# Kernel tuning notes

Measured on AMD Instinct MI355X. Metric: run time of the kernel, lower is better.

## Reference

```python
import jax, jax.numpy as jnp
import numpy as np

B, T, V, F, O, K_ORDER = 16, 16, 512, 64, 64, 3


def setup_inputs() -> dict:
    key = jax.random.key(0)
    k1, k2, k3, k4 = jax.random.split(key, 4)
    x = jax.random.normal(k1, (B, T, V, F), dtype=jnp.float32)
    Att = jax.random.uniform(k2, (B, V, V), dtype=jnp.float32)
    S = jax.random.uniform(k3, (B, T, V, V), dtype=jnp.float32)
    Theta = jax.random.uniform(k4, (K_ORDER, F, O), dtype=jnp.float32) * 0.1
    return {"x": x, "Att": Att, "S": S, "Theta": Theta}


def reference(x, Att, S, Theta):
    # x: (B,T,V,F); Att: (B,V,V); S: (B,T,V,V); Theta: (k,F,O)
    Bv, Tv, Vv, Fv = x.shape
    k_order = Theta.shape[0]
    # symmetrize via elementwise min with transpose over the two vertex dims
    S = jnp.minimum(S, jnp.swapaxes(S, -1, -2))
    # per-timestep: D = diag(sum(A, axis=1)) (sum over rows, i.e. axis=2 here)
    deg = S.sum(axis=2)                      # (B,T,V)
    eye = jnp.eye(Vv, dtype=x.dtype)
    # L_t = D - A - I
    L_t = deg[..., None] * eye - S - eye     # (B,T,V,V)
    Att_b = Att[:, None]                     # (B,1,V,V) broadcast over T

    # Chebyshev recurrence is ELEMENTWISE in the original code: T_k = 2*L_t*T_{k-1} - T_{k-2}
    Tkm2 = jnp.broadcast_to(eye, L_t.shape)  # T_0 = I
    Tkm1 = L_t                               # T_1 = L_t
    # rhs = (T_k * Att)^T @ x  ->  sum_u (T_k*Att)[u,v] * x[u,f]; then @ Theta[k]
    out = jnp.einsum('btuv,btuf,fo->btvo', Tkm2 * Att_b, x, Theta[0])
    if k_order > 1:
        out = out + jnp.einsum('btuv,btuf,fo->btvo', Tkm1 * Att_b, x, Theta[1])
    for i in range(2, k_order):
        Tk = 2.0 * L_t * Tkm1 - Tkm2
        out = out + jnp.einsum('btuv,btuf,fo->btvo', Tk * Att_b, x, Theta[i])
        Tkm2, Tkm1 = Tkm1, Tk
    return jax.nn.relu(out)                  # (B,T,V,O)
```

## Files before the change

kernel.cpp:

```cpp
#include <hip/hip_runtime.h>

#define VV 512
#define FF 64
#define OO 64
#define YELEMS 8388608

#define C1_OFF    0u
#define C2_OFF    67108864u
#define Y1F8_OFF  134217728u
#define Y2F8_OFF  142606336u
#define YVO_OFF   150994944u
#define DEGP_OFF  201326592u
#define SDG_OFF   205520896u
#define ADG_OFF   206045184u
#define WS_NEED   206569472u

using f32x4  = __attribute__((ext_vector_type(4))) float;
using f32x16 = __attribute__((ext_vector_type(16))) float;
using s16x8  = __attribute__((ext_vector_type(8))) short;
using s16x4  = __attribute__((ext_vector_type(4))) short;
using u16x4  = __attribute__((ext_vector_type(4))) unsigned short;
using i64x2  = __attribute__((ext_vector_type(2))) long;

__device__ __forceinline__ short f2bf(float f) {
    union { float f; unsigned int u; } v; v.f = f;
    unsigned int u = v.u;
    u += 0x7fffu + ((u >> 16) & 1u);
    return (short)(u >> 16);
}
__device__ __forceinline__ float bf2f(unsigned short u) {
    union { unsigned int u; float f; } v; v.u = ((unsigned int)u) << 16; return v.f;
}
__device__ __forceinline__ int swz(int row) { return (row >> 1) & 7; }

__device__ __forceinline__ void gload16(const void* g, void* l) {
    __builtin_amdgcn_global_load_lds(
        (const __attribute__((address_space(1))) unsigned int*)g,
        (__attribute__((address_space(3))) unsigned int*)l, 16, 0, 0);
}

__global__ __launch_bounds__(256, 3)
void coef_kernel(const float* __restrict__ S, const float* __restrict__ Att,
                 unsigned char* __restrict__ ws)
{
    __shared__ float Sij[64][65];
    __shared__ float Sji[64][65];
    __shared__ short Aij[64][68];
    __shared__ short Aji[64][68];

    const int tid = threadIdx.x;
    const int bt = blockIdx.x / 36;
    int p = blockIdx.x - bt * 36;
    int i = 0;
    while (p >= 8 - i) { p -= 8 - i; ++i; }
    const int j = i + p;
    const int b = bt >> 4;
    const int u0i = i * 64, u0j = j * 64;

    const float* Sbt = S + (size_t)bt * VV * VV;
    const float* Abt = Att + (size_t)b * VV * VV;

    {
        const int r = tid >> 2, c4 = (tid & 3) * 16;
        const float* gij = Sbt + (size_t)(u0i + r) * VV + u0j + c4;
        const float* gji = Sbt + (size_t)(u0j + r) * VV + u0i + c4;
        const float* aij = Abt + (size_t)(u0i + r) * VV + u0j + c4;
        const float* aji = Abt + (size_t)(u0j + r) * VV + u0i + c4;
        #pragma unroll
        for (int w = 0; w < 4; ++w) {
            float4 t = ((const float4*)gij)[w];
            Sij[r][c4 + w * 4 + 0] = t.x; Sij[r][c4 + w * 4 + 1] = t.y;
            Sij[r][c4 + w * 4 + 2] = t.z; Sij[r][c4 + w * 4 + 3] = t.w;
        }
        #pragma unroll
        for (int w = 0; w < 4; ++w) {
            float4 t = ((const float4*)gji)[w];
            Sji[r][c4 + w * 4 + 0] = t.x; Sji[r][c4 + w * 4 + 1] = t.y;
            Sji[r][c4 + w * 4 + 2] = t.z; Sji[r][c4 + w * 4 + 3] = t.w;
        }
        #pragma unroll
        for (int w = 0; w < 4; ++w) {
            float4 t = ((const float4*)aij)[w];
            s16x4 pk = { f2bf(t.x), f2bf(t.y), f2bf(t.z), f2bf(t.w) };
            *(s16x4*)&Aij[r][c4 + w * 4] = pk;
        }
        #pragma unroll
        for (int w = 0; w < 4; ++w) {
            float4 t = ((const float4*)aji)[w];
            s16x4 pk = { f2bf(t.x), f2bf(t.y), f2bf(t.z), f2bf(t.w) };
            *(s16x4*)&Aji[r][c4 + w * 4] = pk;
        }
    }
    if (i == j && tid < 64) {
        const int vg = u0i + tid;
        ((float*)(ws + SDG_OFF))[(size_t)bt * VV + vg] = Sbt[(size_t)vg * VV + vg];
        ((float*)(ws + ADG_OFF))[(size_t)bt * VV + vg] = Abt[(size_t)vg * VV + vg];
    }
    __syncthreads();

    unsigned char* c1w = ws + C1_OFF + (size_t)bt * (VV * VV);
    unsigned char* c2w = ws + C2_OFF + (size_t)bt * (VV * VV);
    float* degpW = (float*)(ws + DEGP_OFF) + (size_t)bt * 8 * VV;

    const int v  = tid >> 2;
    const int sp = tid & 3;
    const int pr = sp >> 1, idx = sp & 1;

    #pragma unroll
    for (int pass = 0; pass < 2; ++pass) {
        if (pass == 1 && i == j) break;
        const float (*Tuv)[65] = (pass == 0) ? Sij : Sji;
        const float (*Tvu)[65] = (pass == 0) ? Sji : Sij;
        const short (*Auv)[68] = (pass == 0) ? Aij : Aji;
        const int I = (pass == 0) ? i : j;
        const int J = (pass == 0) ? j : i;
        const bool dtile = (i == j);

        float degp = 0.f;
        int w1[4], w2[4];
        #pragma unroll
        for (int t = 0; t < 2; ++t) {
            const int sl = idx * 4 + t * 2 + pr;
            float c1v[8], c2v[8];
            #pragma unroll
            for (int e = 0; e < 8; ++e) {
                const int u = sl * 8 + e;
                float sm = fminf(Tuv[u][v], Tvu[v][u]);
                float a  = bf2f((unsigned short)Auv[u][v]);
                degp += sm;
                float c1 = -a * sm;
                float c2 = (a + a) * (sm * sm);
                if (dtile && (u == v)) { c1 = 0.f; c2 = 0.f; }
                c1v[e] = c1; c2v[e] = c2;
            }
            int a0 = __builtin_amdgcn_cvt_pk_fp8_f32(c1v[0], c1v[1], 0, false);
            a0     = __builtin_amdgcn_cvt_pk_fp8_f32(c1v[2], c1v[3], a0, true);
            int a1 = __builtin_amdgcn_cvt_pk_fp8_f32(c1v[4], c1v[5], 0, false);
            a1     = __builtin_amdgcn_cvt_pk_fp8_f32(c1v[6], c1v[7], a1, true);
            int b0 = __builtin_amdgcn_cvt_pk_fp8_f32(c2v[0], c2v[1], 0, false);
            b0     = __builtin_amdgcn_cvt_pk_fp8_f32(c2v[2], c2v[3], b0, true);
            int b1 = __builtin_amdgcn_cvt_pk_fp8_f32(c2v[4], c2v[5], 0, false);
            b1     = __builtin_amdgcn_cvt_pk_fp8_f32(c2v[6], c2v[7], b1, true);
            w1[t * 2] = a0; w1[t * 2 + 1] = a1;
            w2[t * 2] = b0; w2[t * 2 + 1] = b1;
        }
        const int vglob = J * 64 + v;
        const size_t rowoff = (size_t)vglob * VV + pr * 256 + I * 32 + idx * 16;
        int4 s1 = { w1[0], w1[1], w1[2], w1[3] };
        int4 s2 = { w2[0], w2[1], w2[2], w2[3] };
        *(int4*)(c1w + rowoff) = s1;
        *(int4*)(c2w + rowoff) = s2;

        degp += __shfl_xor(degp, 1);
        degp += __shfl_xor(degp, 2);
        if (sp == 0) degpW[(size_t)I * VV + vglob] = degp;
    }
}

__global__ __launch_bounds__(256, 4)
void y_kernel2(const float* __restrict__ x, const float* __restrict__ Theta,
               unsigned char* __restrict__ ws)
{
    __shared__ __align__(16) unsigned char smem[32768];
    short* xT = (short*)(smem);

    const int tid = threadIdx.x, lane = tid & 63, q = tid >> 6;
    const int g = lane >> 4, nbase = lane & 15;
    const int bt = blockIdx.x >> 3;
    const int u0 = (blockIdx.x & 7) * 64;

    {
        const float* xp = x + ((size_t)(bt * VV + u0 + lane)) * FF + q * 16;
        float4 a0 = ((const float4*)xp)[0];
        float4 a1 = ((const float4*)xp)[1];
        float4 a2 = ((const float4*)xp)[2];
        float4 a3 = ((const float4*)xp)[3];
        float v[16] = {a0.x,a0.y,a0.z,a0.w, a1.x,a1.y,a1.z,a1.w,
                       a2.x,a2.y,a2.z,a2.w, a3.x,a3.y,a3.z,a3.w};
        s16x8 p0, p1;
        #pragma unroll
        for (int e = 0; e < 8; ++e) { p0[e] = f2bf(v[e]); p1[e] = f2bf(v[8 + e]); }
        const int fs = swz(lane);
        *(s16x8*)&xT[lane * 64 + (((q * 2)     ^ fs) * 8)] = p0;
        *(s16x8*)&xT[lane * 64 + (((q * 2 + 1) ^ fs) * 8)] = p1;
    }
    #pragma unroll
    for (int k = 0; k < 3; ++k) {
        short* tk = (short*)(smem + 8192 + k * 8192);
        s16x8 p0, p1;
        #pragma unroll
        for (int e = 0; e < 8; ++e) {
            p0[e] = f2bf(Theta[k * FF * OO + (q * 16 + e) * OO + lane]);
            p1[e] = f2bf(Theta[k * FF * OO + (q * 16 + 8 + e) * OO + lane]);
        }
        const int fs = swz(lane);
        *(s16x8*)&tk[lane * 64 + (((q * 2)     ^ fs) * 8)] = p0;
        *(s16x8*)&tk[lane * 64 + (((q * 2 + 1) ^ fs) * 8)] = p1;
    }
    __syncthreads();

    f32x4 zero = {0.f, 0.f, 0.f, 0.f};
    f32x4 acc[3][4];
    #pragma unroll
    for (int k = 0; k < 3; ++k)
        #pragma unroll
        for (int nt = 0; nt < 4; ++nt) acc[k][nt] = zero;

    const int mrow = q * 16 + nbase;
    const int moff = mrow * 64, ms = swz(mrow);
    #pragma unroll
    for (int kk = 0; kk < 2; ++kk) {
        const int slotA = kk * 4 + g;
        s16x8 a = *(const s16x8*)&xT[moff + ((slotA ^ ms) * 8)];
        #pragma unroll
        for (int nt = 0; nt < 4; ++nt) {
            const int nrow = nt * 16 + nbase;
            const int nad = nrow * 64 + ((slotA ^ swz(nrow)) * 8);
            #pragma unroll
            for (int k = 0; k < 3; ++k) {
                s16x8 bb = *(const s16x8*)&((short*)(smem + 8192 + k * 8192))[nad];
                acc[k][nt] = __builtin_amdgcn_mfma_f32_16x16x32_bf16(a, bb, acc[k][nt], 0, 0, 0);
            }
        }
    }
    unsigned short* yvo = (unsigned short*)(ws + YVO_OFF);
    unsigned char* y1f8 = ws + Y1F8_OFF + (size_t)bt * 32768;
    unsigned char* y2f8 = ws + Y2F8_OFF + (size_t)bt * 32768;
    #pragma unroll
    for (int k = 0; k < 3; ++k) {
        #pragma unroll
        for (int nt = 0; nt < 4; ++nt) {
            const int o = nt * 16 + nbase;
            const int u = u0 + q * 16 + g * 4;
            #pragma unroll
            for (int r = 0; r < 4; ++r)
                yvo[(size_t)k * YELEMS + (size_t)bt * 32768 + (size_t)(u + r) * OO + o] =
                    (unsigned short)f2bf(acc[k][nt][r]);
            if (k >= 1) {
                const int s = u >> 3;
                const int sw = (s & ~15) | ((s & 15) ^ (o & 15));
                const int ad = o * 512 + sw * 8 + (u & 4);
                int w = __builtin_amdgcn_cvt_pk_fp8_f32(acc[k][nt][0], acc[k][nt][1], 0, false);
                w     = __builtin_amdgcn_cvt_pk_fp8_f32(acc[k][nt][2], acc[k][nt][3], w, true);
                if (k == 1) *(int*)(y1f8 + ad) = w;
                else        *(int*)(y2f8 + ad) = w;
            }
        }
    }
}

__global__ __launch_bounds__(256, 2)
void cheb_b(const unsigned char* __restrict__ ws, float* __restrict__ out)
{
    __shared__ __align__(16) unsigned char yLds[65536];

    const int tid = threadIdx.x, lane = tid & 63;
    const int wv = tid >> 6;
    const int vh = wv >> 1, oh = wv & 1;
    const int rl = lane & 31, hi = lane >> 5;

    const int wg = blockIdx.x;
    const int bt = (wg & 7) + ((wg >> 6) << 3);
    const int vt = (wg >> 3) & 7;
    const int v0 = vt * 64;

    {
        const unsigned char* y1img = ws + Y1F8_OFF + (size_t)bt * 32768;
        const unsigned char* y2img = ws + Y2F8_OFF + (size_t)bt * 32768;
        const int wo = wv * 1024 + lane * 16;
        #pragma unroll
        for (int i = 0; i < 8; ++i) {
            gload16(y1img + i * 4096 + wo, (char*)yLds + i * 4096 + wv * 1024);
            gload16(y2img + i * 4096 + wo, (char*)yLds + 32768 + i * 4096 + wv * 1024);
        }
    }

    const size_t crow = (size_t)(v0 + vh * 32 + rl) * VV + hi * 256;
    const unsigned char* c1base = ws + C1_OFF + (size_t)bt * (VV * VV) + crow;
    const unsigned char* c2base = ws + C2_OFF + (size_t)bt * (VV * VV) + crow;
    i64x2 c1p[16], c2p[16];
    #pragma unroll
    for (int jj = 0; jj < 16; ++jj) {
        c1p[jj] = *(const i64x2*)(c1base + jj * 16);
        c2p[jj] = *(const i64x2*)(c2base + jj * 16);
    }

    __syncthreads();

    f32x16 acc;
    #pragma unroll
    for (int i = 0; i < 16; ++i) acc[i] = 0.f;

    const int yrow = (oh * 32 + rl) * 512;
    const int x15  = rl & 15;

    #pragma unroll
    for (int it = 0; it < 32; ++it) {
        const long a1 = c1p[it >> 1][it & 1];
        const long a2 = c2p[it >> 1][it & 1];
        const int s  = it * 2 + hi;
        const int sw = (s & ~15) | ((s & 15) ^ x15);
        const int ad = yrow + sw * 8;
        const long b1 = *(const long*)&yLds[ad];
        const long b2 = *(const long*)&yLds[32768 + ad];
        acc = __builtin_amdgcn_mfma_f32_32x32x16_fp8_fp8(a1, b1, acc, 0, 0, 0);
        acc = __builtin_amdgcn_mfma_f32_32x32x16_fp8_fp8(a2, b2, acc, 0, 0, 0);
    }

    __syncthreads();
    {
        float* ep = (float*)yLds;
        const float* degp = (const float*)(ws + DEGP_OFF) + (size_t)bt * 8 * VV;
        const float* SdgW = (const float*)(ws + SDG_OFF) + (size_t)bt * VV;
        const float* AdgW = (const float*)(ws + ADG_OFF) + (size_t)bt * VV;
        if (tid < 64) {
            float dv = 0.f;
            #pragma unroll
            for (int s = 0; s < 8; ++s) dv += degp[(size_t)s * VV + v0 + tid];
            ep[tid] = dv;
        } else if (tid < 128) {
            ep[64 + (tid - 64)] = SdgW[v0 + (tid - 64)];
        } else if (tid < 192) {
            ep[128 + (tid - 128)] = AdgW[v0 + (tid - 128)];
        }
    }
    __syncthreads();

    const float* ep = (const float*)yLds;
    const unsigned short* yvo = (const unsigned short*)(ws + YVO_OFF) + (size_t)bt * 32768;
    float* obt = out + (size_t)bt * VV * OO;
    const int o = oh * 32 + rl;

    #pragma unroll
    for (int r = 0; r < 16; ++r) {
        const int vloc = vh * 32 + (r & 3) + 8 * (r >> 2) + 4 * hi;
        const int vgr = v0 + vloc;
        const float dv = ep[vloc];
        const float Sd = ep[64 + vloc];
        const float Ad = ep[128 + vloc];
        const float Ld = dv - Sd - 1.0f;
        const float w1 = Ad * Ld;
        const float w2 = Ad * (2.0f * Ld * Ld - 1.0f);
        const size_t yi = (size_t)vgr * OO + o;
        float y0v = bf2f(yvo[yi]);
        float y1v = bf2f(yvo[(size_t)YELEMS + yi]);
        float y2v = bf2f(yvo[(size_t)2 * YELEMS + yi]);
        float val = acc[r] + Ad * y0v + w1 * y1v + w2 * y2v;
        obt[(size_t)vgr * OO + o] = fmaxf(val, 0.0f);
    }
}

__global__ __launch_bounds__(256, 4)
void y_kernel_fb(const float* __restrict__ x, const float* __restrict__ Theta,
                 unsigned short* __restrict__ yT)
{
    __shared__ __align__(16) unsigned char smem[32768];
    short* xT = (short*)(smem);
    const int tid = threadIdx.x, lane = tid & 63, q = tid >> 6;
    const int g = lane >> 4, nbase = lane & 15;
    const int bt = blockIdx.x >> 3;
    const int u0 = (blockIdx.x & 7) * 64;
    {
        const float* xp = x + ((size_t)(bt * VV + u0 + lane)) * FF + q * 16;
        float4 a0 = ((const float4*)xp)[0];
        float4 a1 = ((const float4*)xp)[1];
        float4 a2 = ((const float4*)xp)[2];
        float4 a3 = ((const float4*)xp)[3];
        float v[16] = {a0.x,a0.y,a0.z,a0.w, a1.x,a1.y,a1.z,a1.w,
                       a2.x,a2.y,a2.z,a2.w, a3.x,a3.y,a3.z,a3.w};
        s16x8 p0, p1;
        #pragma unroll
        for (int e = 0; e < 8; ++e) { p0[e] = f2bf(v[e]); p1[e] = f2bf(v[8 + e]); }
        const int fs = swz(lane);
        *(s16x8*)&xT[lane * 64 + (((q * 2)     ^ fs) * 8)] = p0;
        *(s16x8*)&xT[lane * 64 + (((q * 2 + 1) ^ fs) * 8)] = p1;
    }
    #pragma unroll
    for (int k = 0; k < 3; ++k) {
        short* tk = (short*)(smem + 8192 + k * 8192);
        s16x8 p0, p1;
        #pragma unroll
        for (int e = 0; e < 8; ++e) {
            p0[e] = f2bf(Theta[k * FF * OO + (q * 16 + e) * OO + lane]);
            p1[e] = f2bf(Theta[k * FF * OO + (q * 16 + 8 + e) * OO + lane]);
        }
        const int fs = swz(lane);
        *(s16x8*)&tk[lane * 64 + (((q * 2)     ^ fs) * 8)] = p0;
        *(s16x8*)&tk[lane * 64 + (((q * 2 + 1) ^ fs) * 8)] = p1;
    }
    __syncthreads();
    f32x4 zero = {0.f, 0.f, 0.f, 0.f};
    f32x4 acc[3][4];
    #pragma unroll
    for (int k = 0; k < 3; ++k)
        #pragma unroll
        for (int nt = 0; nt < 4; ++nt) acc[k][nt] = zero;
    const int mrow = q * 16 + nbase;
    const int moff = mrow * 64, ms = swz(mrow);
    #pragma unroll
    for (int kk = 0; kk < 2; ++kk) {
        const int slotA = kk * 4 + g;
        s16x8 a = *(const s16x8*)&xT[moff + ((slotA ^ ms) * 8)];
        #pragma unroll
        for (int nt = 0; nt < 4; ++nt) {
            const int nrow = nt * 16 + nbase;
            const int nad = nrow * 64 + ((slotA ^ swz(nrow)) * 8);
            #pragma unroll
            for (int k = 0; k < 3; ++k) {
                s16x8 bb = *(const s16x8*)&((short*)(smem + 8192 + k * 8192))[nad];
                acc[k][nt] = __builtin_amdgcn_mfma_f32_16x16x32_bf16(a, bb, acc[k][nt], 0, 0, 0);
            }
        }
    }
    #pragma unroll
    for (int k = 0; k < 3; ++k) {
        #pragma unroll
        for (int nt = 0; nt < 4; ++nt) {
            const int o = nt * 16 + nbase;
            const int u = u0 + q * 16 + g * 4;
            u16x4 pk;
            #pragma unroll
            for (int r = 0; r < 4; ++r) pk[r] = (unsigned short)f2bf(acc[k][nt][r]);
            *(u16x4*)&yT[(size_t)k * YELEMS + ((size_t)(bt * 64 + o)) * VV + u] = pk;
        }
    }
}

__global__ __launch_bounds__(256, 4)
void cheb_main_fb(const float* __restrict__ S, const float* __restrict__ Att,
                  const unsigned short* __restrict__ yT, float* __restrict__ out)
{
    const int tid = threadIdx.x, lane = tid & 63, q = tid >> 6;
    const int g = lane >> 4, nbase = lane & 15;
    const int wg = blockIdx.x;
    const int bt = (wg & 7) + ((wg >> 6) << 3);
    const int vt = (wg >> 3) & 7;
    const int v0 = vt * 64;
    const int b  = bt >> 4;
    const float* Sbt = S + (size_t)bt * VV * VV;
    const float* Abt = Att + (size_t)b * VV * VV;
    const unsigned short* y0g = yT + (size_t)bt * 64 * VV;
    const unsigned short* y1g = y0g + (size_t)YELEMS;
    const unsigned short* y2g = y0g + (size_t)2 * YELEMS;
    const int mrow = q * 16 + nbase;
    const int vg   = v0 + mrow;
    const float* Srow = Sbt + (size_t)vg * VV;
    const float* Scol = Sbt + vg;
    const float* Acol = Abt + vg;
    f32x4 zero = {0.f, 0.f, 0.f, 0.f};
    f32x4 acc[4];
    #pragma unroll
    for (int i = 0; i < 4; ++i) acc[i] = zero;
    float da0 = 0.f, da1 = 0.f, adg = 0.f, sdg = 0.f;
    #pragma unroll
    for (int ut = 0; ut < 8; ++ut) {
        const int u0t = ut * 64;
        #pragma unroll
        for (int kk = 0; kk < 2; ++kk) {
            const int ub = u0t + (kk * 4 + g) * 8;
            s16x8 b10 = *(const s16x8*)&y1g[(size_t)(0 * 16 + nbase) * VV + ub];
            s16x8 b11 = *(const s16x8*)&y1g[(size_t)(1 * 16 + nbase) * VV + ub];
            s16x8 b12 = *(const s16x8*)&y1g[(size_t)(2 * 16 + nbase) * VV + ub];
            s16x8 b13 = *(const s16x8*)&y1g[(size_t)(3 * 16 + nbase) * VV + ub];
            f32x4 r0 = *(const f32x4*)(Srow + ub);
            f32x4 r1 = *(const f32x4*)(Srow + ub + 4);
            s16x8 a1, a2;
            #pragma unroll
            for (int e = 0; e < 8; ++e) {
                float sc = Scol[(size_t)(ub + e) * VV];
                float av = Acol[(size_t)(ub + e) * VV];
                float rv = (e < 4) ? r0[e] : r1[e - 4];
                float sm = fminf(sc, rv);
                if (e & 1) da1 += sm; else da0 += sm;
                float c1 = -av * sm;
                float c2 = (av + av) * (sm * sm);
                if (ub + e == vg) { c1 = 0.f; c2 = 0.f; adg = av; sdg = sm; }
                a1[e] = f2bf(c1);
                a2[e] = f2bf(c2);
            }
            acc[0] = __builtin_amdgcn_mfma_f32_16x16x32_bf16(a1, b10, acc[0], 0, 0, 0);
            acc[1] = __builtin_amdgcn_mfma_f32_16x16x32_bf16(a1, b11, acc[1], 0, 0, 0);
            acc[2] = __builtin_amdgcn_mfma_f32_16x16x32_bf16(a1, b12, acc[2], 0, 0, 0);
            acc[3] = __builtin_amdgcn_mfma_f32_16x16x32_bf16(a1, b13, acc[3], 0, 0, 0);
            s16x8 b20 = *(const s16x8*)&y2g[(size_t)(0 * 16 + nbase) * VV + ub];
            s16x8 b21 = *(const s16x8*)&y2g[(size_t)(1 * 16 + nbase) * VV + ub];
            s16x8 b22 = *(const s16x8*)&y2g[(size_t)(2 * 16 + nbase) * VV + ub];
            s16x8 b23 = *(const s16x8*)&y2g[(size_t)(3 * 16 + nbase) * VV + ub];
            acc[0] = __builtin_amdgcn_mfma_f32_16x16x32_bf16(a2, b20, acc[0], 0, 0, 0);
            acc[1] = __builtin_amdgcn_mfma_f32_16x16x32_bf16(a2, b21, acc[1], 0, 0, 0);
            acc[2] = __builtin_amdgcn_mfma_f32_16x16x32_bf16(a2, b22, acc[2], 0, 0, 0);
            acc[3] = __builtin_amdgcn_mfma_f32_16x16x32_bf16(a2, b23, acc[3], 0, 0, 0);
        }
    }
    float da = da0 + da1;
    da  += __shfl_xor(da, 16);  da  += __shfl_xor(da, 32);
    adg += __shfl_xor(adg, 16); adg += __shfl_xor(adg, 32);
    sdg += __shfl_xor(sdg, 16); sdg += __shfl_xor(sdg, 32);
    float* obt = out + (size_t)bt * VV * OO;
    #pragma unroll
    for (int r = 0; r < 4; ++r) {
        const int vloc = q * 16 + g * 4 + r;
        const int src  = g * 4 + r;
        const float Ad = __shfl(adg, src);
        const float dv = __shfl(da,  src);
        const float Sd = __shfl(sdg, src);
        const float Ld = dv - Sd - 1.0f;
        const float w1 = Ad * Ld;
        const float w2 = Ad * (2.0f * Ld * Ld - 1.0f);
        const int vgr = v0 + vloc;
        #pragma unroll
        for (int nt = 0; nt < 4; ++nt) {
            const int oo = nt * 16 + nbase;
            const size_t yi = (size_t)oo * VV + vgr;
            float y0v = bf2f(y0g[yi]);
            float y1v = bf2f(y1g[yi]);
            float y2v = bf2f(y2g[yi]);
            float val = acc[nt][r] + Ad * y0v + w1 * y1v + w2 * y2v;
            obt[(size_t)vgr * OO + oo] = fmaxf(val, 0.0f);
        }
    }
}

extern "C" void kernel_launch(void* const* d_in, const int* in_sizes, int n_in,
                              void* d_out, int out_size, void* d_ws, size_t ws_size,
                              hipStream_t stream) {
    (void)in_sizes; (void)n_in; (void)out_size;
    const float* x   = (const float*)d_in[0];
    const float* Att = (const float*)d_in[1];
    const float* S   = (const float*)d_in[2];
    const float* Th  = (const float*)d_in[3];
    float* outp = (float*)d_out;
    if (ws_size >= (size_t)WS_NEED) {
        unsigned char* ws = (unsigned char*)d_ws;
        hipLaunchKernelGGL(coef_kernel, dim3(9216), dim3(256), 0, stream, S, Att, ws);
        hipLaunchKernelGGL(y_kernel2, dim3(2048), dim3(256), 0, stream, x, Th, ws);
        hipLaunchKernelGGL(cheb_b, dim3(2048), dim3(256), 0, stream, ws, outp);
    } else {
        unsigned short* yT = (unsigned short*)d_ws;
        hipLaunchKernelGGL(y_kernel_fb, dim3(2048), dim3(256), 0, stream, x, Th, yT);
        hipLaunchKernelGGL(cheb_main_fb, dim3(2048), dim3(256), 0, stream, S, Att, yT, outp);
    }
}
```

Before: 214.5 us.

## Precompute transposed bf16 Att per batch in a separate kernel

Adds att_kernel, which converts Att to bf16 once per batch and stores it transposed in the workspace. coef_kernel then reads the needed row directly instead of loading and converting two fp32 Att tiles for every (b,t) block. This removes T-fold redundant Att traffic and shrinks coef_kernel's shared memory, and its launch bounds are raised to 4 blocks to use the higher occupancy. The cost is an extra kernel launch, and the transposed Att is staged in the Y1F8 workspace region, which must not be overwritten before coef_kernel reads it.

```diff
diff --git a/kernel.cpp b/kernel.cpp
--- a/kernel.cpp
+++ b/kernel.cpp
@@ -39,14 +39,42 @@
         (__attribute__((address_space(3))) unsigned int*)l, 16, 0, 0);
 }
 
-__global__ __launch_bounds__(256, 3)
+__global__ __launch_bounds__(256, 4)
+void att_kernel(const float* __restrict__ Att, unsigned char* __restrict__ ws)
+{
+    __shared__ float T[64][65];
+    const int tid = threadIdx.x;
+    const int b  = blockIdx.x >> 6;
+    const int ij = blockIdx.x & 63;
+    const int i = ij >> 3, j = ij & 7;
+    const float* Ab = Att + (size_t)b * VV * VV;
+    const int r = tid >> 2, c4 = (tid & 3) * 16;
+    const float* src = Ab + (size_t)(i * 64 + r) * VV + j * 64 + c4;
+    #pragma unroll
+    for (int w = 0; w < 4; ++w) {
+        float4 t = ((const float4*)src)[w];
+        T[r][c4 + w * 4 + 0] = t.x; T[r][c4 + w * 4 + 1] = t.y;
+        T[r][c4 + w * 4 + 2] = t.z; T[r][c4 + w * 4 + 3] = t.w;
+    }
+    __syncthreads();
+    unsigned short* dst = (unsigned short*)(ws + Y1F8_OFF) + (size_t)b * (VV * VV)
+                        + (size_t)(j * 64 + r) * VV + i * 64 + c4;
+    s16x8 p0, p1;
+    #pragma unroll
+    for (int e = 0; e < 8; ++e) {
+        p0[e] = f2bf(T[c4 + e][r]);
+        p1[e] = f2bf(T[c4 + 8 + e][r]);
+    }
+    *(s16x8*)dst = p0;
+    *(s16x8*)(dst + 8) = p1;
+}
+
+__global__ __launch_bounds__(256, 4)
 void coef_kernel(const float* __restrict__ S, const float* __restrict__ Att,
                  unsigned char* __restrict__ ws)
 {
     __shared__ float Sij[64][65];
     __shared__ float Sji[64][65];
-    __shared__ short Aij[64][68];
-    __shared__ short Aji[64][68];
 
     const int tid = threadIdx.x;
     const int bt = blockIdx.x / 36;
@@ -59,13 +87,12 @@
 
     const float* Sbt = S + (size_t)bt * VV * VV;
     const float* Abt = Att + (size_t)b * VV * VV;
+    const unsigned short* atT = (const unsigned short*)(ws + Y1F8_OFF) + (size_t)b * (VV * VV);
 
     {
         const int r = tid >> 2, c4 = (tid & 3) * 16;
         const float* gij = Sbt + (size_t)(u0i + r) * VV + u0j + c4;
         const float* gji = Sbt + (size_t)(u0j + r) * VV + u0i + c4;
-        const float* aij = Abt + (size_t)(u0i + r) * VV + u0j + c4;
-        const float* aji = Abt + (size_t)(u0j + r) * VV + u0i + c4;
         #pragma unroll
         for (int w = 0; w < 4; ++w) {
             float4 t = ((const float4*)gij)[w];
@@ -78,18 +105,6 @@
             Sji[r][c4 + w * 4 + 0] = t.x; Sji[r][c4 + w * 4 + 1] = t.y;
             Sji[r][c4 + w * 4 + 2] = t.z; Sji[r][c4 + w * 4 + 3] = t.w;
         }
-        #pragma unroll
-        for (int w = 0; w < 4; ++w) {
-            float4 t = ((const float4*)aij)[w];
-            s16x4 pk = { f2bf(t.x), f2bf(t.y), f2bf(t.z), f2bf(t.w) };
-            *(s16x4*)&Aij[r][c4 + w * 4] = pk;
-        }
-        #pragma unroll
-        for (int w = 0; w < 4; ++w) {
-            float4 t = ((const float4*)aji)[w];
-            s16x4 pk = { f2bf(t.x), f2bf(t.y), f2bf(t.z), f2bf(t.w) };
-            *(s16x4*)&Aji[r][c4 + w * 4] = pk;
-        }
     }
     if (i == j && tid < 64) {
         const int vg = u0i + tid;
@@ -111,22 +126,24 @@
         if (pass == 1 && i == j) break;
         const float (*Tuv)[65] = (pass == 0) ? Sij : Sji;
         const float (*Tvu)[65] = (pass == 0) ? Sji : Sij;
-        const short (*Auv)[68] = (pass == 0) ? Aij : Aji;
         const int I = (pass == 0) ? i : j;
         const int J = (pass == 0) ? j : i;
         const bool dtile = (i == j);
 
+        const unsigned short* arow = atT + (size_t)(J * 64 + v) * VV + I * 64;
+
         float degp = 0.f;
         int w1[4], w2[4];
         #pragma unroll
         for (int t = 0; t < 2; ++t) {
             const int sl = idx * 4 + t * 2 + pr;
+            s16x8 a8 = *(const s16x8*)(arow + sl * 8);
             float c1v[8], c2v[8];
             #pragma unroll
             for (int e = 0; e < 8; ++e) {
                 const int u = sl * 8 + e;
                 float sm = fminf(Tuv[u][v], Tvu[v][u]);
-                float a  = bf2f((unsigned short)Auv[u][v]);
+                float a  = bf2f((unsigned short)a8[e]);
                 degp += sm;
                 float c1 = -a * sm;
                 float c2 = (a + a) * (sm * sm);
@@ -532,6 +549,7 @@
     float* outp = (float*)d_out;
     if (ws_size >= (size_t)WS_NEED) {
         unsigned char* ws = (unsigned char*)d_ws;
+        hipLaunchKernelGGL(att_kernel, dim3(1024), dim3(256), 0, stream, Att, ws);
         hipLaunchKernelGGL(coef_kernel, dim3(9216), dim3(256), 0, stream, S, Att, ws);
         hipLaunchKernelGGL(y_kernel2, dim3(2048), dim3(256), 0, stream, x, Th, ws);
         hipLaunchKernelGGL(cheb_b, dim3(2048), dim3(256), 0, stream, ws, outp);
```

Result: slower. 224.0 us (+4.4%).
